# Kernel tuning notes

Hardware: AMD Instinct MI355X
Metric: run time of the kernel (lower is better)

## Reference

```python
import jax, jax.numpy as jnp
import numpy as np

B, S, D, L, R = 8, 128, 512, 512, 50  # batch, seq_len, input_dim, linear_dim, n_rel_labels


def _head_params(key, n_out):
    k1, k2, k3, k4 = jax.random.split(key, 4)
    s1 = 1.0 / np.sqrt(2 * D)
    s2 = 1.0 / np.sqrt(L)
    return (jax.random.uniform(k1, (2 * D, L), jnp.float32, -s1, s1),
            jax.random.uniform(k2, (L,), jnp.float32, -s1, s1),
            jax.random.uniform(k3, (L, n_out), jnp.float32, -s2, s2),
            jax.random.uniform(k4, (n_out,), jnp.float32, -s2, s2))


def setup_inputs() -> dict:
    key = jax.random.key(0)
    kx, ks, kh, kt, kl = jax.random.split(key, 5)
    x = jax.random.normal(kx, (B, S, D), jnp.float32)
    span = _head_params(ks, 1)
    h2h = _head_params(kh, 1)
    t2t = _head_params(kt, 1)
    lab = _head_params(kl, R)
    return {
        'x': x,
        'span_W1': span[0], 'span_b1': span[1], 'span_W2': span[2], 'span_b2': span[3],
        'h2h_W1': h2h[0], 'h2h_b1': h2h[1], 'h2h_W2': h2h[2], 'h2h_b2': h2h[3],
        't2t_W1': t2t[0], 't2t_b1': t2t[1], 't2t_W2': t2t[2], 't2t_b2': t2t[3],
        'lab_W1': lab[0], 'lab_b1': lab[1], 'lab_W2': lab[2], 'lab_b2': lab[3],
    }


def _pair_head(x, W1, b1, W2, b2):
    # Linear on concat([x_i, x_j]) == x_i @ W_left + x_j @ W_right  (avoids [B,S,S,2D] concat)
    d = x.shape[-1]
    Wl, Wr = W1[:d], W1[d:]
    left = jnp.einsum('bid,dl->bil', x, Wl)   # [B,S,L]
    right = jnp.einsum('bjd,dl->bjl', x, Wr)  # [B,S,L]
    h = jnp.tanh(left[:, :, None, :] + right[:, None, :, :] + b1)  # [B,S,S,L]
    return jnp.einsum('bijl,lo->bijo', h, W2) + b2  # [B,S,S,n_out]


def reference(x, span_W1, span_b1, span_W2, span_b2,
              h2h_W1, h2h_b1, h2h_W2, h2h_b2,
              t2t_W1, t2t_b1, t2t_W2, t2t_b2,
              lab_W1, lab_b1, lab_W2, lab_b2):
    shst = _pair_head(x, span_W1, span_b1, span_W2, span_b2)[..., 0]  # [B,S,S]
    # torch: movedim(-1,1) -> triu + triu(1).T -> movedim(1,-1)
    bt = jnp.swapaxes(shst, 1, 2)
    sym = jnp.triu(bt) + jnp.swapaxes(jnp.triu(bt, 1), -1, -2)
    shst = jnp.swapaxes(sym, 1, 2)
    shoh = _pair_head(x, h2h_W1, h2h_b1, h2h_W2, h2h_b2)[..., 0]
    stot = _pair_head(x, t2t_W1, t2t_b1, t2t_W2, t2t_b2)[..., 0]
    shoh_labels = _pair_head(x, lab_W1, lab_b1, lab_W2, lab_b2)  # [B,S,S,R]
    return (shst, shoh, stot, shoh_labels)
```

## Files before the change

kernel.cpp:

```cpp
#include <hip/hip_runtime.h>

#define Bsz 8
#define Ssz 128
#define Dsz 512
#define D2 1024
#define Lsz 512
#define Rsz 50
#define SLOT 524288
#define BSLOT 65536
#define OUTMAT 131072

typedef __attribute__((ext_vector_type(8))) _Float16 f16x8;
typedef __attribute__((ext_vector_type(2))) __fp16 fp16x2;
typedef __attribute__((ext_vector_type(4))) float f32x4;

union UV4 { uint4 u; f16x8 h; };
union UH { unsigned short s; _Float16 h; };
union UP { fp16x2 h; unsigned u; };

struct K1Args {
  const float* W1[4];
  const float* b1[4];
};

__device__ __forceinline__ float f16lo(unsigned u) {
  UH x; x.s = (unsigned short)(u & 0xffffu); return (float)x.h;
}
__device__ __forceinline__ float f16hi(unsigned u) {
  UH x; x.s = (unsigned short)(u >> 16); return (float)x.h;
}
__device__ __forceinline__ float f16v(unsigned short s) {
  UH x; x.s = s; return (float)x.h;
}
__device__ __forceinline__ unsigned pkrtz(float a, float b) {
  UP c; c.h = __builtin_amdgcn_cvt_pkrtz(a, b); return c.u;
}
__device__ __forceinline__ unsigned short f2h(float v) {
  UH x; x.h = (_Float16)v; return x.s;
}
__device__ __forceinline__ float rcpf(float x) {
  return __builtin_amdgcn_rcpf(x);
}

__device__ __forceinline__ unsigned tanh2u(unsigned ea, unsigned eb) {
  UP a, b, p; a.u = ea; b.u = eb;
  const fp16x2 one = {(__fp16)1.0f, (__fp16)1.0f};
  p.h = a.h * b.h + one;
  const float h0 = fmaf(-2.0f, rcpf((float)p.h.x), 1.0f);
  const float h1 = fmaf(-2.0f, rcpf((float)p.h.y), 1.0f);
  return pkrtz(h0, h1);
}

__global__ __launch_bounds__(256) void prep_all(
    const float* __restrict__ x, K1Args a, const float* __restrict__ W2,
    const float* __restrict__ w2a, const float* __restrict__ w2b,
    const float* __restrict__ w2c,
    const float* __restrict__ b2a, const float* __restrict__ b2b,
    const float* __restrict__ b2c,
    unsigned short* __restrict__ W1F, unsigned short* __restrict__ X16F,
    unsigned short* __restrict__ W2F, float* __restrict__ Sums) {
  const int z = blockIdx.z;
  const int t = threadIdx.x;
  if (z < 4) {
    if (blockIdx.x >= 8) return;
    __shared__ float S[64][65];
    const float* __restrict__ W = a.W1[z];
    const int n0 = blockIdx.x * 64;
    const int k0 = blockIdx.y * 64;
    {
      const int kk = t >> 2, c16 = (t & 3) * 16;
      const float* p = W + (k0 + kk) * Lsz + n0 + c16;
#pragma unroll
      for (int c = 0; c < 4; ++c) {
        float4 v = *(const float4*)(p + c * 4);
        S[kk][c16 + c * 4 + 0] = v.x; S[kk][c16 + c * 4 + 1] = v.y;
        S[kk][c16 + c * 4 + 2] = v.z; S[kk][c16 + c * 4 + 3] = v.w;
      }
    }
    __syncthreads();
#pragma unroll
    for (int o = t; o < 512; o += 256) {
      const int lane = o & 63;
      const int ntl = (o >> 6) & 3, kbl = o >> 8;
      const int n_l = ntl * 16 + (lane & 15);
      const int k_l = kbl * 32 + (lane >> 4) * 8;
      uint4 pk;
      pk.x = pkrtz(S[k_l + 0][n_l], S[k_l + 1][n_l]);
      pk.y = pkrtz(S[k_l + 2][n_l], S[k_l + 3][n_l]);
      pk.z = pkrtz(S[k_l + 4][n_l], S[k_l + 5][n_l]);
      pk.w = pkrtz(S[k_l + 6][n_l], S[k_l + 7][n_l]);
      const long addr =
          ((long)((z * 32 + blockIdx.x * 4 + ntl) * 32 + blockIdx.y * 2 + kbl) *
               64 + lane) * 8;
      *(uint4*)(W1F + addr) = pk;
    }
  } else if (z == 4) {
    if (blockIdx.x >= 16) return;
    const int idx = (blockIdx.y * 16 + blockIdx.x) * 256 + t;
    const int frag = idx >> 6, lane = idx & 63;
    const int m = (frag >> 4) * 16 + (lane & 15);
    const int k0 = (frag & 15) * 32 + (lane >> 4) * 8;
    const float* p = x + m * Dsz + k0;
    float4 v0 = *(const float4*)p, v1 = *(const float4*)(p + 4);
    uint4 pk = make_uint4(pkrtz(v0.x, v0.y), pkrtz(v0.z, v0.w),
                          pkrtz(v1.x, v1.y), pkrtz(v1.z, v1.w));
    *(uint4*)(X16F + (long)idx * 8) = pk;
  } else {
    if (blockIdx.y != 0) return;
    if (blockIdx.x < 16) {
      const int idx = blockIdx.x * 256 + t;
      const int frag = idx >> 6, lane = idx & 63;
      const int o = (frag >> 4) * 16 + (lane & 15);
      const int k0 = (frag & 15) * 32 + (lane >> 4) * 8;
      float v[8];
#pragma unroll
      for (int e = 0; e < 8; ++e)
        v[e] = (o < Rsz) ? W2[(k0 + e) * Rsz + o] : 0.0f;
      uint4 pk = make_uint4(pkrtz(v[0], v[1]), pkrtz(v[2], v[3]),
                            pkrtz(v[4], v[5]), pkrtz(v[6], v[7]));
      *(uint4*)(W2F + (long)idx * 8) = pk;
    } else if (blockIdx.x < 19) {
      const int h = blockIdx.x - 16;
      const float* __restrict__ w2 = (h == 0) ? w2a : (h == 1 ? w2b : w2c);
      const float bb = (h == 0) ? b2a[0] : (h == 1 ? b2b[0] : b2c[0]);
      __shared__ float red[256];
      red[t] = w2[t] + w2[t + 256];
      __syncthreads();
      for (int s = 128; s > 0; s >>= 1) {
        if (t < s) red[t] += red[t + s];
        __syncthreads();
      }
      if (t == 0) Sums[h] = red[0] + bb;
    }
  }
}

__global__ __launch_bounds__(256) void gemm_lr_f16f(
    const unsigned short* __restrict__ X16F,
    const unsigned short* __restrict__ W1F, K1Args a,
    unsigned short* __restrict__ U) {
  const int side = blockIdx.z;
  const int h = side >> 1, r = side & 1;
  const float* __restrict__ bias = a.b1[h];
  const int tid = threadIdx.x;
  const int w = tid >> 6, lane = tid & 63;
  const int lm = lane & 15, q = lane >> 4;
  const int mtb = blockIdx.y * 4 + (w & 1) * 2;
  const int ntb = blockIdx.x * 4 + (w >> 1) * 2;

  f32x4 acc[2][2];
#pragma unroll
  for (int mt = 0; mt < 2; ++mt)
#pragma unroll
    for (int nt = 0; nt < 2; ++nt) {
      acc[mt][nt].x = 0.f; acc[mt][nt].y = 0.f;
      acc[mt][nt].z = 0.f; acc[mt][nt].w = 0.f;
    }

  for (int kb = 0; kb < 16; ++kb) {
    UV4 af[2], bf[2];
#pragma unroll
    for (int mt = 0; mt < 2; ++mt)
      af[mt].u = *(const uint4*)(X16F +
          ((long)((mtb + mt) * 16 + kb) * 64 + lane) * 8);
#pragma unroll
    for (int nt = 0; nt < 2; ++nt)
      bf[nt].u = *(const uint4*)(W1F +
          ((long)((h * 32 + ntb + nt) * 32 + r * 16 + kb) * 64 + lane) * 8);
#pragma unroll
    for (int mt = 0; mt < 2; ++mt)
#pragma unroll
      for (int nt = 0; nt < 2; ++nt)
        acc[mt][nt] = __builtin_amdgcn_mfma_f32_16x16x32_f16(
            af[mt].h, bf[nt].h, acc[mt][nt], 0, 0, 0);
  }

  unsigned short* slot = U + side * SLOT;
  if (h < 3) {
#pragma unroll
    for (int nt = 0; nt < 2; ++nt) {
      const int n_out = (ntb + nt) * 16 + lm;
      const float bb = (r == 0) ? bias[n_out] : 0.0f;
#pragma unroll
      for (int mt = 0; mt < 2; ++mt) {
        const int m0r = (mtb + mt) * 16 + q * 4;
        const float e0 = __expf(2.0f * (acc[mt][nt].x + bb));
        const float e1 = __expf(2.0f * (acc[mt][nt].y + bb));
        const float e2 = __expf(2.0f * (acc[mt][nt].z + bb));
        const float e3 = __expf(2.0f * (acc[mt][nt].w + bb));
        uint2 pr;
        pr.x = pkrtz(e0, e1);
        pr.y = pkrtz(e2, e3);
        const int bi = m0r >> 7, il = m0r & 127;
        *(uint2*)(slot + bi * BSLOT + n_out * Ssz + il) = pr;
      }
    }
  } else {
#pragma unroll
    for (int nt = 0; nt < 2; ++nt) {
      const int n_out = (ntb + nt) * 16 + lm;
      const float bb = (r == 0) ? bias[n_out] : 0.0f;
#pragma unroll
      for (int mt = 0; mt < 2; ++mt) {
#pragma unroll
        for (int reg = 0; reg < 4; ++reg) {
          const int m_out = (mtb + mt) * 16 + q * 4 + reg;
          float v;
          if (reg == 0) v = acc[mt][nt].x;
          else if (reg == 1) v = acc[mt][nt].y;
          else if (reg == 2) v = acc[mt][nt].z;
          else v = acc[mt][nt].w;
          slot[m_out * Lsz + n_out] = f2h(__expf(2.0f * (v + bb)));
        }
      }
    }
  }
}

__global__ __launch_bounds__(256) void pair_fused(
    const unsigned short* __restrict__ U,
    const unsigned short* __restrict__ W2F,
    const float* __restrict__ b2l,
    const float* __restrict__ w2a, const float* __restrict__ w2b,
    const float* __restrict__ w2c,
    float* __restrict__ P, float* __restrict__ out) {
  __shared__ unsigned short As[64][20];
  __shared__ unsigned short Bs[64][40];
  __shared__ float w2s[64];

  const int b = blockIdx.y;
  const int tid = threadIdx.x;

  if (blockIdx.x >= 192) {
    const int i = blockIdx.x - 192;
    const int w = tid >> 6, lane = tid & 63;
    const int lm = lane & 15, q = lane >> 4;
    const int jb = w * 32;

    const unsigned short* __restrict__ Lrow =
        U + 6 * SLOT + (b * Ssz + i) * Lsz;
    const unsigned short* __restrict__ Rb0 = U + 7 * SLOT + (long)b * Ssz * Lsz;
    float* out3 = out + 3 * OUTMAT;

    const unsigned short* Lb = Lrow + q * 8;
    const unsigned short* R0 = Rb0 + (jb + lm) * Lsz + q * 8;
    const unsigned short* R1 = Rb0 + (jb + 16 + lm) * Lsz + q * 8;
    const unsigned short* Bb = W2F + lane * 8;

    f32x4 acc[2][4];
#pragma unroll
    for (int mt = 0; mt < 2; ++mt)
#pragma unroll
      for (int nt = 0; nt < 4; ++nt) {
        acc[mt][nt].x = 0.f; acc[mt][nt].y = 0.f;
        acc[mt][nt].z = 0.f; acc[mt][nt].w = 0.f;
      }

#pragma unroll 2
    for (int c = 0; c < 8; ++c) {
      const uint4 lf0 = *(const uint4*)(Lb + c * 64);
      const uint4 lf1 = *(const uint4*)(Lb + c * 64 + 32);
#pragma unroll
      for (int kbl = 0; kbl < 2; ++kbl) {
        const uint4 lf = kbl ? lf1 : lf0;
        UV4 bfr[4];
#pragma unroll
        for (int nt = 0; nt < 4; ++nt)
          bfr[nt].u =
              *(const uint4*)(Bb + (long)(nt * 16 + kbl + 2 * c) * 512);
#pragma unroll
        for (int mt = 0; mt < 2; ++mt) {
          const uint4 rv =
              *(const uint4*)((mt ? R1 : R0) + c * 64 + kbl * 32);
          UV4 A;
          A.u = make_uint4(tanh2u(lf.x, rv.x), tanh2u(lf.y, rv.y),
                           tanh2u(lf.z, rv.z), tanh2u(lf.w, rv.w));
#pragma unroll
          for (int nt = 0; nt < 4; ++nt)
            acc[mt][nt] = __builtin_amdgcn_mfma_f32_16x16x32_f16(
                A.h, bfr[nt].h, acc[mt][nt], 0, 0, 0);
        }
      }
    }

#pragma unroll
    for (int nt = 0; nt < 4; ++nt) {
      const int o = nt * 16 + lm;
      if (o >= Rsz) continue;
      const float bias = b2l[o];
#pragma unroll
      for (int mt = 0; mt < 2; ++mt) {
#pragma unroll
        for (int reg = 0; reg < 4; ++reg) {
          const int j = jb + mt * 16 + q * 4 + reg;
          const long base = ((long)((b * Ssz + i) * Ssz) + j) * Rsz;
          float v;
          if (reg == 0) v = acc[mt][nt].x;
          else if (reg == 1) v = acc[mt][nt].y;
          else if (reg == 2) v = acc[mt][nt].z;
          else v = acc[mt][nt].w;
          out3[base + o] = v + bias;
        }
      }
    }
  } else {
    const int tile = blockIdx.x >> 1;
    const int lhalf = blockIdx.x & 1;
    const int h = tile >> 5;
    const int r = tile & 31;
    const int it = r >> 2, jt = r & 3;
    const int i0 = it * 16, j0 = jt * 32;
    if (h == 0 && i0 + 15 < j0) return;
    const int t = tid;
    const int tj = t & 31;
    const int th = t >> 5;
    const int lb = lhalf * 256;

    const unsigned short* __restrict__ A  = U + (2 * h) * SLOT + b * BSLOT;
    const unsigned short* __restrict__ Bt = U + (2 * h + 1) * SLOT + b * BSLOT;
    const float* __restrict__ w2 = (h == 0) ? w2a : (h == 1 ? w2b : w2c);

    float acc0 = 0.f, acc1 = 0.f;
    const int sr = t >> 2;
    const int scA = (t & 3) * 4;
    const int scB = (t & 3) * 8;

    for (int lc = lb; lc < lb + 256; lc += 64) {
      __syncthreads();
      *(uint2*)&As[sr][scA] = *(const uint2*)(A + (lc + sr) * Ssz + i0 + scA);
      *(uint4*)&Bs[sr][scB] = *(const uint4*)(Bt + (lc + sr) * Ssz + j0 + scB);
      if (t < 64) w2s[t] = w2[lc + t];
      __syncthreads();
#pragma unroll 8
      for (int l = 0; l < 64; ++l) {
        const float wv = w2s[l];
        const unsigned ua = *(const unsigned*)&As[l][th * 2];
        const float a0 = f16lo(ua), a1 = f16hi(ua);
        const float bb = f16v(Bs[l][tj]);
        acc0 = fmaf(wv, rcpf(fmaf(a0, bb, 1.0f)), acc0);
        acc1 = fmaf(wv, rcpf(fmaf(a1, bb, 1.0f)), acc1);
      }
    }

    const int i = i0 + th * 2, j = j0 + tj;
    float* Ph = P + ((long)(lhalf * 3 + h) * Bsz + b) * 16384;
    Ph[i * Ssz + j] = acc0;
    Ph[(i + 1) * Ssz + j] = acc1;
  }
}

__global__ __launch_bounds__(256) void combine_sc(
    const float* __restrict__ P, const float* __restrict__ Sums,
    float* __restrict__ out) {
  const int ck = blockIdx.x, b = blockIdx.y, h = blockIdx.z;
  const int t = threadIdx.x;
  const float Sh = Sums[h];
  const float* P0 = P + ((long)(0 * 3 + h) * Bsz + b) * 16384;
  const float* P1 = P + ((long)(1 * 3 + h) * Bsz + b) * 16384;
  if (h == 0) {
#pragma unroll
    for (int k = 0; k < 8; ++k) {
      const int idx = ck * 2048 + k * 256 + t;
      const int i = idx >> 7, j = idx & 127;
      if (j > i) continue;
      const float v = fmaf(-2.0f, P0[idx] + P1[idx], Sh);
      out[(b * Ssz + i) * Ssz + j] = v;
      out[(b * Ssz + j) * Ssz + i] = v;
    }
  } else {
    float* o = out + h * OUTMAT + b * 16384;
#pragma unroll
    for (int k = 0; k < 8; ++k) {
      const int idx = ck * 2048 + k * 256 + t;
      o[idx] = fmaf(-2.0f, P0[idx] + P1[idx], Sh);
    }
  }
}

extern "C" void kernel_launch(void* const* d_in, const int* in_sizes, int n_in,
                              void* d_out, int out_size, void* d_ws,
                              size_t ws_size, hipStream_t stream) {
  (void)in_sizes; (void)n_in; (void)out_size; (void)ws_size;
  const float* x = (const float*)d_in[0];
  K1Args a;
  a.W1[0] = (const float*)d_in[1];  a.b1[0] = (const float*)d_in[2];
  a.W1[1] = (const float*)d_in[5];  a.b1[1] = (const float*)d_in[6];
  a.W1[2] = (const float*)d_in[9];  a.b1[2] = (const float*)d_in[10];
  a.W1[3] = (const float*)d_in[13]; a.b1[3] = (const float*)d_in[14];
  const float* w2a = (const float*)d_in[3];
  const float* b2a = (const float*)d_in[4];
  const float* w2b = (const float*)d_in[7];
  const float* b2b = (const float*)d_in[8];
  const float* w2c = (const float*)d_in[11];
  const float* b2c = (const float*)d_in[12];
  const float* W2l = (const float*)d_in[15];
  const float* b2l = (const float*)d_in[16];
  float* out = (float*)d_out;

  unsigned short* U    = (unsigned short*)d_ws;
  unsigned short* W1F  = U + 8 * SLOT;
  unsigned short* X16F = U + 8 * SLOT + 4 * (Lsz * D2);
  unsigned short* W2F  = U + 8 * SLOT + 5 * (Lsz * D2);
  float* Sums = (float*)(W2F + 64 * Lsz);
  float* P = Sums + 4;

  prep_all<<<dim3(19, 16, 6), 256, 0, stream>>>(
      x, a, W2l, w2a, w2b, w2c, b2a, b2b, b2c, W1F, X16F, W2F, Sums);
  gemm_lr_f16f<<<dim3(8, 16, 8), 256, 0, stream>>>(X16F, W1F, a, U);
  pair_fused<<<dim3(320, Bsz), 256, 0, stream>>>(
      U, W2F, b2l, w2a, w2b, w2c, P, out);
  combine_sc<<<dim3(8, Bsz, 3), 256, 0, stream>>>(P, Sums, out);
}
```

Before: 166.2 us.

## Store scalar-head exp activations row-major and use packed fp16 pair math

The prep kernel now writes all heads' exp(2*u) values in row-major [row, L] layout rather than transposing the three scalar heads to [L, S]. The pair kernel loads a whole 256-wide L slice for its 16x32 tile into LDS at once, which drops the per-64-chunk sync loop. The inner loop now uses vector LDS reads and packed fp16 multiply-add (a*b+1) for two elements at a time before the reciprocal. This trades the earlier per-element widening and fp32 fma for fp16 products, which lowers precision and adds strided scalar 16-bit stores in prep and a larger LDS footprint.

```diff
diff --git a/kernel.cpp b/kernel.cpp
--- a/kernel.cpp
+++ b/kernel.cpp
@@ -7,7 +7,6 @@
 #define Lsz 512
 #define Rsz 50
 #define SLOT 524288
-#define BSLOT 65536
 #define OUTMAT 131072
 
 typedef __attribute__((ext_vector_type(8))) _Float16 f16x8;
@@ -23,15 +22,6 @@
   const float* b1[4];
 };
 
-__device__ __forceinline__ float f16lo(unsigned u) {
-  UH x; x.s = (unsigned short)(u & 0xffffu); return (float)x.h;
-}
-__device__ __forceinline__ float f16hi(unsigned u) {
-  UH x; x.s = (unsigned short)(u >> 16); return (float)x.h;
-}
-__device__ __forceinline__ float f16v(unsigned short s) {
-  UH x; x.s = s; return (float)x.h;
-}
 __device__ __forceinline__ unsigned pkrtz(float a, float b) {
   UP c; c.h = __builtin_amdgcn_cvt_pkrtz(a, b); return c.u;
 }
@@ -49,6 +39,16 @@
   const float h0 = fmaf(-2.0f, rcpf((float)p.h.x), 1.0f);
   const float h1 = fmaf(-2.0f, rcpf((float)p.h.y), 1.0f);
   return pkrtz(h0, h1);
+}
+
+__device__ __forceinline__ float pk2(unsigned a, unsigned b, float wlo,
+                                     float whi, float acc) {
+  UP pa, pb, pp; pa.u = a; pb.u = b;
+  const fp16x2 one = {(__fp16)1.0f, (__fp16)1.0f};
+  pp.h = pa.h * pb.h + one;
+  acc = fmaf(wlo, rcpf((float)pp.h.x), acc);
+  acc = fmaf(whi, rcpf((float)pp.h.y), acc);
+  return acc;
 }
 
 __global__ __launch_bounds__(256) void prep_all(
@@ -176,42 +176,21 @@
   }
 
   unsigned short* slot = U + side * SLOT;
-  if (h < 3) {
-#pragma unroll
-    for (int nt = 0; nt < 2; ++nt) {
-      const int n_out = (ntb + nt) * 16 + lm;
-      const float bb = (r == 0) ? bias[n_out] : 0.0f;
-#pragma unroll
-      for (int mt = 0; mt < 2; ++mt) {
-        const int m0r = (mtb + mt) * 16 + q * 4;
-        const float e0 = __expf(2.0f * (acc[mt][nt].x + bb));
-        const float e1 = __expf(2.0f * (acc[mt][nt].y + bb));
-        const float e2 = __expf(2.0f * (acc[mt][nt].z + bb));
-        const float e3 = __expf(2.0f * (acc[mt][nt].w + bb));
-        uint2 pr;
-        pr.x = pkrtz(e0, e1);
-        pr.y = pkrtz(e2, e3);
-        const int bi = m0r >> 7, il = m0r & 127;
-        *(uint2*)(slot + bi * BSLOT + n_out * Ssz + il) = pr;
-      }
-    }
-  } else {
-#pragma unroll
-    for (int nt = 0; nt < 2; ++nt) {
-      const int n_out = (ntb + nt) * 16 + lm;
-      const float bb = (r == 0) ? bias[n_out] : 0.0f;
-#pragma unroll
-      for (int mt = 0; mt < 2; ++mt) {
-#pragma unroll
-        for (int reg = 0; reg < 4; ++reg) {
-          const int m_out = (mtb + mt) * 16 + q * 4 + reg;
-          float v;
-          if (reg == 0) v = acc[mt][nt].x;
-          else if (reg == 1) v = acc[mt][nt].y;
-          else if (reg == 2) v = acc[mt][nt].z;
-          else v = acc[mt][nt].w;
-          slot[m_out * Lsz + n_out] = f2h(__expf(2.0f * (v + bb)));
-        }
+#pragma unroll
+  for (int nt = 0; nt < 2; ++nt) {
+    const int n_out = (ntb + nt) * 16 + lm;
+    const float bb = (r == 0) ? bias[n_out] : 0.0f;
+#pragma unroll
+    for (int mt = 0; mt < 2; ++mt) {
+#pragma unroll
+      for (int reg = 0; reg < 4; ++reg) {
+        const int m_out = (mtb + mt) * 16 + q * 4 + reg;
+        float v;
+        if (reg == 0) v = acc[mt][nt].x;
+        else if (reg == 1) v = acc[mt][nt].y;
+        else if (reg == 2) v = acc[mt][nt].z;
+        else v = acc[mt][nt].w;
+        slot[m_out * Lsz + n_out] = f2h(__expf(2.0f * (v + bb)));
       }
     }
   }
@@ -224,9 +203,9 @@
     const float* __restrict__ w2a, const float* __restrict__ w2b,
     const float* __restrict__ w2c,
     float* __restrict__ P, float* __restrict__ out) {
-  __shared__ unsigned short As[64][20];
-  __shared__ unsigned short Bs[64][40];
-  __shared__ float w2s[64];
+  __shared__ unsigned short As[16][264];
+  __shared__ unsigned short Bs[32][264];
+  __shared__ float w2s[256];
 
   const int b = blockIdx.y;
   const int tid = threadIdx.x;
@@ -313,36 +292,54 @@
     if (h == 0 && i0 + 15 < j0) return;
     const int t = tid;
     const int tj = t & 31;
-    const int th = t >> 5;
+    const int th2 = (t >> 5) * 2;
     const int lb = lhalf * 256;
 
-    const unsigned short* __restrict__ A  = U + (2 * h) * SLOT + b * BSLOT;
-    const unsigned short* __restrict__ Bt = U + (2 * h + 1) * SLOT + b * BSLOT;
+    const unsigned short* __restrict__ A =
+        U + (2 * h) * SLOT + (long)(b * Ssz + i0) * Lsz + lb;
+    const unsigned short* __restrict__ Bt =
+        U + (2 * h + 1) * SLOT + (long)(b * Ssz + j0) * Lsz + lb;
     const float* __restrict__ w2 = (h == 0) ? w2a : (h == 1 ? w2b : w2c);
 
+    {
+      const int ar = t >> 4, ao = (t & 15) * 16;
+      const uint4 va0 = *(const uint4*)(A + ar * Lsz + ao);
+      const uint4 va1 = *(const uint4*)(A + ar * Lsz + ao + 8);
+      const int br = t >> 3, bo = (t & 7) * 32;
+      const uint4 vb0 = *(const uint4*)(Bt + br * Lsz + bo);
+      const uint4 vb1 = *(const uint4*)(Bt + br * Lsz + bo + 8);
+      const uint4 vb2 = *(const uint4*)(Bt + br * Lsz + bo + 16);
+      const uint4 vb3 = *(const uint4*)(Bt + br * Lsz + bo + 24);
+      const float wv = w2[lb + t];
+      *(uint4*)&As[ar][ao]     = va0;
+      *(uint4*)&As[ar][ao + 8] = va1;
+      *(uint4*)&Bs[br][bo]      = vb0;
+      *(uint4*)&Bs[br][bo + 8]  = vb1;
+      *(uint4*)&Bs[br][bo + 16] = vb2;
+      *(uint4*)&Bs[br][bo + 24] = vb3;
+      w2s[t] = wv;
+    }
+    __syncthreads();
+
     float acc0 = 0.f, acc1 = 0.f;
-    const int sr = t >> 2;
-    const int scA = (t & 3) * 4;
-    const int scB = (t & 3) * 8;
-
-    for (int lc = lb; lc < lb + 256; lc += 64) {
-      __syncthreads();
-      *(uint2*)&As[sr][scA] = *(const uint2*)(A + (lc + sr) * Ssz + i0 + scA);
-      *(uint4*)&Bs[sr][scB] = *(const uint4*)(Bt + (lc + sr) * Ssz + j0 + scB);
-      if (t < 64) w2s[t] = w2[lc + t];
-      __syncthreads();
-#pragma unroll 8
-      for (int l = 0; l < 64; ++l) {
-        const float wv = w2s[l];
-        const unsigned ua = *(const unsigned*)&As[l][th * 2];
-        const float a0 = f16lo(ua), a1 = f16hi(ua);
-        const float bb = f16v(Bs[l][tj]);
-        acc0 = fmaf(wv, rcpf(fmaf(a0, bb, 1.0f)), acc0);
-        acc1 = fmaf(wv, rcpf(fmaf(a1, bb, 1.0f)), acc1);
-      }
-    }
-
-    const int i = i0 + th * 2, j = j0 + tj;
+#pragma unroll 4
+    for (int l = 0; l < 256; l += 8) {
+      const uint4 a0 = *(const uint4*)&As[th2][l];
+      const uint4 a1 = *(const uint4*)&As[th2 + 1][l];
+      const uint4 bv = *(const uint4*)&Bs[tj][l];
+      const float4 w0 = *(const float4*)&w2s[l];
+      const float4 w1 = *(const float4*)&w2s[l + 4];
+      acc0 = pk2(a0.x, bv.x, w0.x, w0.y, acc0);
+      acc0 = pk2(a0.y, bv.y, w0.z, w0.w, acc0);
+      acc0 = pk2(a0.z, bv.z, w1.x, w1.y, acc0);
+      acc0 = pk2(a0.w, bv.w, w1.z, w1.w, acc0);
+      acc1 = pk2(a1.x, bv.x, w0.x, w0.y, acc1);
+      acc1 = pk2(a1.y, bv.y, w0.z, w0.w, acc1);
+      acc1 = pk2(a1.z, bv.z, w1.x, w1.y, acc1);
+      acc1 = pk2(a1.w, bv.w, w1.z, w1.w, acc1);
+    }
+
+    const int i = i0 + th2, j = j0 + tj;
     float* Ph = P + ((long)(lhalf * 3 + h) * Bsz + b) * 16384;
     Ph[i * Ssz + j] = acc0;
     Ph[(i + 1) * Ssz + j] = acc1;
```

Measured after the change: 173.7 us. +4.5%, slower.
